# Optimization experiments

Hardware: AMD Instinct MI355X
Metric: run time of the kernel (lower is better)

The kernel has to match this reference:

```python
import jax, jax.numpy as jnp
import numpy as np

H = 16        # num_attention_heads
G = 16        # groups
SCALE_MIN = 0.95
SCALE_MAX = 1.05


def setup_inputs() -> dict:
    key = jax.random.key(0)
    ks = jax.random.split(key, 9)
    B, S, E = 2, 2048, 1024
    d = {
        'hidden_states': jax.random.normal(ks[0], (B, S, E), jnp.float32),
        'Wq': jax.random.normal(ks[1], (E, E), jnp.float32) * (E ** -0.5),
        'bq': jax.random.normal(ks[2], (E,), jnp.float32) * 0.02,
        'Wk': jax.random.normal(ks[3], (E, E), jnp.float32) * (E ** -0.5),
        'bk': jax.random.normal(ks[4], (E,), jnp.float32) * 0.02,
        'Wv': jax.random.normal(ks[5], (E, E), jnp.float32) * (E ** -0.5),
        'bv': jax.random.normal(ks[6], (E,), jnp.float32) * 0.02,
        'Ws': jax.random.normal(ks[7], (H * G, E), jnp.float32) * (E ** -0.5),
        'bs': jax.random.normal(ks[8], (H * G,), jnp.float32) * 0.02,
    }
    return d


def _shape_heads(x, B, S):
    # [B,S,h*D] -> [B,h,S,D]
    return x.reshape(B, S, H, -1).transpose(0, 2, 1, 3)


def reference(hidden_states, Wq, bq, Wk, bk, Wv, bv, Ws, bs):
    B, S, E = hidden_states.shape
    D = E // H            # head dim = 64
    gd = D // G           # group dim = 4

    Q = _shape_heads(hidden_states @ Wq.T + bq, B, S)   # [B,h,S,D]
    K = _shape_heads(hidden_states @ Wk.T + bk, B, S)
    V = _shape_heads(hidden_states @ Wv.T + bv, B, S)

    # groupwise dynamic scales, narrow sigmoid range
    s_logits = hidden_states @ Ws.T + bs                 # [B,S,h*g]
    s = jax.nn.sigmoid(s_logits) * (SCALE_MAX - SCALE_MIN) + SCALE_MIN
    s = s.reshape(B, S, H, G).transpose(0, 2, 1, 3)      # [B,h,S,g]
    s = jnp.repeat(s, gd, axis=-1)                       # [B,h,S,D]

    Q = Q * s  # apply_to='q'

    scores = jnp.einsum('bhsd,bhtd->bhst', Q, K) / jnp.sqrt(jnp.float32(D))
    probs = jax.nn.softmax(scores, axis=-1)
    ctx = jnp.einsum('bhst,bhtd->bhsd', probs, V)        # [B,h,S,D]
    ctx = ctx.transpose(0, 2, 1, 3).reshape(B, S, H * D)
    return ctx
```

## Files before the change

### kernel.cpp

```cpp
#include <hip/hip_runtime.h>

typedef short bf16x8 __attribute__((ext_vector_type(8)));
typedef float f32x4 __attribute__((ext_vector_type(4)));

__device__ inline float bf2f(ushort u) {
    unsigned v = ((unsigned)u) << 16;
    return __builtin_bit_cast(float, v);
}
__device__ inline ushort f2bf(float f) {
    unsigned u = __builtin_bit_cast(unsigned, f);
    u += 0x7fffu + ((u >> 16) & 1u);
    return (ushort)(u >> 16);
}
__device__ inline void async_load16(const ushort* g, ushort* l) {
    __builtin_amdgcn_global_load_lds((const __attribute__((address_space(1))) void*)g,
                                     (__attribute__((address_space(3))) void*)l, 16, 0, 0);
}

__global__ void cast_all(const float* __restrict__ hs, const float* __restrict__ Wq,
                         const float* __restrict__ Wk, const float* __restrict__ Wv,
                         const float* __restrict__ Ws,
                         ushort* __restrict__ dhs, ushort* __restrict__ dWq,
                         ushort* __restrict__ dWk, ushort* __restrict__ dWv,
                         ushort* __restrict__ dWs)
{
    int bid = blockIdx.x;
    const float* src; ushort* dst; int off;
    if (bid < 2048)      { src = hs; dst = dhs; off = bid; }
    else if (bid < 2560) { src = Wq; dst = dWq; off = bid - 2048; }
    else if (bid < 3072) { src = Wk; dst = dWk; off = bid - 2560; }
    else if (bid < 3584) { src = Wv; dst = dWv; off = bid - 3072; }
    else                 { src = Ws; dst = dWs; off = bid - 3584; }
    int i = (off * 256 + threadIdx.x) * 8;
    float4 a = *(const float4*)(src + i);
    float4 b = *(const float4*)(src + i + 4);
    union { ushort u[8]; float4 v; } o;
    o.u[0] = f2bf(a.x); o.u[1] = f2bf(a.y); o.u[2] = f2bf(a.z); o.u[3] = f2bf(a.w);
    o.u[4] = f2bf(b.x); o.u[5] = f2bf(b.y); o.u[6] = f2bf(b.z); o.u[7] = f2bf(b.w);
    *(float4*)(dst + i) = o.v;
}

__launch_bounds__(256, 4)
__global__ void fused_qkvs(const ushort* __restrict__ X,
                           const ushort* __restrict__ Wq, const ushort* __restrict__ Wk,
                           const ushort* __restrict__ Wv, const ushort* __restrict__ Ws,
                           const float* __restrict__ bq, const float* __restrict__ bk,
                           const float* __restrict__ bv, const float* __restrict__ bs,
                           ushort* __restrict__ Qb, ushort* __restrict__ Kb,
                           ushort* __restrict__ VtG, float* __restrict__ sb)
{
    __shared__ __align__(16) ushort Sm[128 * 136];
    ushort* As = Sm;
    ushort* Bs = Sm + 128 * 64;

    const int tid = threadIdx.x, w = tid >> 6, lane = tid & 63;
    const int l15 = lane & 15, quad = lane >> 4;
    const int lrow = lane >> 3;
    const int gchunk = ((lane & 7) ^ lrow) * 8;

    const int wid = blockIdx.x;
    const int r8 = wid & 7, jj = wid >> 3;
    const int by = (jj & 3) * 8 + r8;
    const int xb = jj >> 2;
    const int m0 = by * 128;

    const ushort* W; const float* bias; int n0, mode;
    if (xb < 8)       { W = Wq; bias = bq; n0 = xb * 128;        mode = 1; }
    else if (xb < 16) { W = Wk; bias = bk; n0 = (xb - 8) * 128;  mode = 0; }
    else if (xb < 24) { W = Wv; bias = bv; n0 = (xb - 16) * 128; mode = 2; }
    else              { W = Ws; bias = bs; n0 = (xb - 24) * 128; mode = 3; }

    const int wm = (w >> 1) * 64, wn = (w & 1) * 64;

    f32x4 acc[4][4];
    for (int i = 0; i < 4; i++) for (int j = 0; j < 4; j++) acc[i][j] = (f32x4){0.f, 0.f, 0.f, 0.f};

    for (int k0 = 0; k0 < 1024; k0 += 64) {
        __syncthreads();
        for (int c = 0; c < 4; ++c) {
            int r = w * 32 + c * 8;
            async_load16(&X[(size_t)(m0 + r + lrow) * 1024 + k0 + gchunk], &As[r * 64]);
            async_load16(&W[(size_t)(n0 + r + lrow) * 1024 + k0 + gchunk], &Bs[r * 64]);
        }
        __syncthreads();
        for (int kk = 0; kk < 64; kk += 32) {
            const int csw = quad + (kk >> 3);
            bf16x8 a[4], b[4];
            for (int i = 0; i < 4; i++)
                a[i] = *(const bf16x8*)&As[(wm + i * 16 + l15) * 64 + ((csw ^ (l15 & 7)) * 8)];
            for (int j = 0; j < 4; j++)
                b[j] = *(const bf16x8*)&Bs[(wn + j * 16 + l15) * 64 + ((csw ^ (l15 & 7)) * 8)];
            for (int i = 0; i < 4; i++)
                for (int j = 0; j < 4; j++)
                    acc[i][j] = __builtin_amdgcn_mfma_f32_16x16x32_bf16(a[i], b[j], acc[i][j], 0, 0, 0);
        }
    }

    const float QSCALE = 0.125f * 1.44269504f;

    if (mode == 3) {
        for (int i = 0; i < 4; i++)
            for (int j = 0; j < 4; j++) {
                int gn = n0 + wn + j * 16 + l15;
                float bv_ = bias[gn];
                for (int r = 0; r < 4; r++) {
                    int gm = m0 + wm + i * 16 + quad * 4 + r;
                    float v = acc[i][j][r] + bv_;
                    float sg = __builtin_amdgcn_rcpf(1.0f + __builtin_amdgcn_exp2f(-v * 1.44269504f));
                    sb[(size_t)gm * 256 + gn] = sg * 0.1f + 0.95f;
                }
            }
        return;
    }

    __syncthreads();

    if (mode == 2) {
        for (int i = 0; i < 4; i++)
            for (int j = 0; j < 4; j++) {
                int gnl = wn + j * 16 + l15;
                float bv_ = bias[n0 + gnl];
                ushort4 pk;
                pk.x = f2bf(acc[i][j][0] + bv_);
                pk.y = f2bf(acc[i][j][1] + bv_);
                pk.z = f2bf(acc[i][j][2] + bv_);
                pk.w = f2bf(acc[i][j][3] + bv_);
                *(ushort4*)&Sm[gnl * 136 + wm + i * 16 + quad * 4] = pk;
            }
        __syncthreads();
        const int bb = m0 >> 11, sloc = m0 & 2047;
        for (int it = 0; it < 8; ++it) {
            int d = (tid >> 4) + it * 16;
            int s8 = (tid & 15) * 8;
            float4 v = *(float4*)&Sm[d * 136 + s8];
            int h = (n0 + d) >> 6, dd = d & 63;
            *(float4*)&VtG[(size_t)(bb * 16 + h) * 131072 + (size_t)dd * 2048 + sloc + s8] = v;
        }
    } else {
        for (int i = 0; i < 4; i++)
            for (int j = 0; j < 4; j++) {
                int gnl = wn + j * 16 + l15;
                float bv_ = bias[n0 + gnl];
                for (int r = 0; r < 4; r++) {
                    float v = acc[i][j][r] + bv_;
                    if (mode == 1) v *= QSCALE;
                    Sm[(wm + i * 16 + quad * 4 + r) * 136 + gnl] = f2bf(v);
                }
            }
        __syncthreads();
        ushort* dst = (mode == 1) ? Qb : Kb;
        for (int it = 0; it < 8; ++it) {
            int row = (tid >> 4) + it * 16, c = (tid & 15) * 8;
            *(float4*)&dst[(size_t)(m0 + row) * 1024 + n0 + c] = *(float4*)&Sm[row * 136 + c];
        }
    }
}

__launch_bounds__(128, 2)
__global__ void attn_kernel(const ushort* __restrict__ Q, const ushort* __restrict__ K,
                            const ushort* __restrict__ Vt, const float* __restrict__ sb,
                            float* __restrict__ out)
{
    __shared__ __align__(16) ushort SmA[4 * 4096];
    __shared__ __align__(16) ushort Ps[2048];
    ushort* Ks0 = SmA;
    ushort* Ks1 = SmA + 4096;
    ushort* Vs0 = SmA + 8192;
    ushort* Vs1 = SmA + 12288;
    ushort* Qs  = SmA + 4096;

    const int tid = threadIdx.x, w = tid >> 6, lane = tid & 63;
    const int l15 = lane & 15, quad = lane >> 4;
    const int lrow = lane >> 3;
    const int gchunk = ((lane & 7) ^ lrow) * 8;

    const int wid = blockIdx.x;
    const int r8 = wid & 7, jj = wid >> 3;
    const int bh = (jj & 3) * 8 + r8;
    const int qx = jj >> 2;
    const int b = bh >> 4, h = bh & 15;
    const int q0 = qx * 64;
    const size_t rowbase = (size_t)b * 2048;
    const int cbase = h * 64;

    const ushort* kg = K + (rowbase + w * 32 + lrow) * 1024 + cbase + gchunk;
    const ushort* vg = Vt + (size_t)bh * 131072 + (size_t)(w * 32 + lrow) * 2048 + gchunk;

    for (int c = 0; c < 4; ++c) {
        async_load16(kg + c * 8192,  Ks0 + w * 2048 + c * 512);
        async_load16(vg + c * 16384, Vs0 + w * 2048 + c * 512);
    }

    for (int it = 0; it < 4; ++it) {
        int l = tid + it * 128;
        int r = l >> 3, ch = l & 7;
        int c = ch * 8;
        union { float4 f; ushort u[8]; } uu, oo;
        uu.f = *(const float4*)&Q[(rowbase + q0 + r) * 1024 + cbase + c];
        const float* sp = &sb[(rowbase + q0 + r) * 256 + ((cbase + c) >> 2)];
        float s0 = sp[0], s1 = sp[1];
        for (int j = 0; j < 4; j++) oo.u[j] = f2bf(bf2f(uu.u[j]) * s0);
        for (int j = 4; j < 8; j++) oo.u[j] = f2bf(bf2f(uu.u[j]) * s1);
        *(float4*)&Qs[r * 64 + ((ch ^ (r & 7)) * 8)] = oo.f;
    }
    __syncthreads();

    bf16x8 aq[2][2];
    for (int mt = 0; mt < 2; mt++)
        for (int kk2 = 0; kk2 < 2; kk2++)
            aq[mt][kk2] = *(const bf16x8*)&Qs[(w * 32 + mt * 16 + l15) * 64
                                              + (((kk2 * 4 + quad) ^ (l15 & 7)) * 8)];

    int kvoff[2][4];
    for (int kk2 = 0; kk2 < 2; kk2++)
        for (int nt = 0; nt < 4; nt++)
            kvoff[kk2][nt] = (nt * 16 + l15) * 64 + (((quad + kk2 * 4) ^ (l15 & 7)) * 8);
    int wroff2[4], rdoff2[2];
    {
        const int base = w * 1024 + l15 * 64;
        for (int kt2 = 0; kt2 < 4; kt2++)
            wroff2[kt2] = base + (quad & 1) * 4 + (((kt2 * 2 + (quad >> 1)) ^ (l15 & 7)) * 8);
        for (int half = 0; half < 2; half++)
            rdoff2[half] = base + (((half * 4 + quad) ^ (l15 & 7)) * 8);
    }

    const bf16x8 vones = {0x3F80, 0x3F80, 0x3F80, 0x3F80, 0x3F80, 0x3F80, 0x3F80, 0x3F80};

    f32x4 osum[2];
    f32x4 o[2][4];
    for (int mt = 0; mt < 2; mt++) {
        osum[mt] = (f32x4){0.f, 0.f, 0.f, 0.f};
        for (int nt = 0; nt < 4; nt++) o[mt][nt] = (f32x4){0.f, 0.f, 0.f, 0.f};
    }
    const f32x4 z4 = (f32x4){0.f, 0.f, 0.f, 0.f};

#define ATTN_STEP(KC, VC, KN, VN, KT, PREFETCH)                                                         \
    {                                                                                                   \
        __syncthreads();                  \
        if (PREFETCH) {                                                                                 \
            const int nk = (KT) + 1;                                                                    \
            for (int c = 0; c < 4; ++c) {                                                               \
                async_load16(kg + nk * 65536 + c * 8192, KN + w * 2048 + c * 512);                      \
                async_load16(vg + nk * 64 + c * 16384,   VN + w * 2048 + c * 512);                      \
            }                                                                                           \
        }                                                                                               \
        bf16x8 kb[2][4], vb[2][4];                                                                      \
        for (int kk2 = 0; kk2 < 2; kk2++)                                                               \
            for (int nt = 0; nt < 4; nt++) {                                                            \
                kb[kk2][nt] = *(const bf16x8*)&KC[kvoff[kk2][nt]];                                      \
                vb[kk2][nt] = *(const bf16x8*)&VC[kvoff[kk2][nt]];                                      \
            }                                                                                           \
        for (int mt = 0; mt < 2; mt++) {                                                                \
                                                     \
            f32x4 st[4];                                                                                \
            __builtin_amdgcn_s_setprio(1);                                                              \
            for (int kt2 = 0; kt2 < 4; kt2++) {                                                         \
                st[kt2] = __builtin_amdgcn_mfma_f32_16x16x32_bf16(kb[0][kt2], aq[mt][0], z4, 0, 0, 0);  \
                st[kt2] = __builtin_amdgcn_mfma_f32_16x16x32_bf16(kb[1][kt2], aq[mt][1], st[kt2],       \
                                                                  0, 0, 0);                             \
            }                                                                                           \
            __builtin_amdgcn_s_setprio(0);                                                              \
            for (int kt2 = 0; kt2 < 4; kt2++) {                                                         \
                float p0 = __builtin_amdgcn_exp2f(st[kt2][0]);                                          \
                float p1 = __builtin_amdgcn_exp2f(st[kt2][1]);                                          \
                float p2 = __builtin_amdgcn_exp2f(st[kt2][2]);                                          \
                float p3 = __builtin_amdgcn_exp2f(st[kt2][3]);                                          \
                unsigned d0 = __builtin_amdgcn_perm(__builtin_bit_cast(unsigned, p1) + 0x8000u,         \
                                                    __builtin_bit_cast(unsigned, p0) + 0x8000u,         \
                                                    0x07060302u);                                       \
                unsigned d1 = __builtin_amdgcn_perm(__builtin_bit_cast(unsigned, p3) + 0x8000u,         \
                                                    __builtin_bit_cast(unsigned, p2) + 0x8000u,         \
                                                    0x07060302u);                                       \
                uint2 pk; pk.x = d0; pk.y = d1;                                                         \
                *(uint2*)&Ps[wroff2[kt2]] = pk;                                                         \
            }                                                                                           \
                           \
            __builtin_amdgcn_s_setprio(1);                                                              \
            for (int half = 0; half < 2; half++) {                                                      \
                bf16x8 a_ = *(const bf16x8*)&Ps[rdoff2[half]];                                          \
                osum[mt] = __builtin_amdgcn_mfma_f32_16x16x32_bf16(a_, vones, osum[mt], 0, 0, 0);       \
                for (int nt = 0; nt < 4; nt++)                                                          \
                    o[mt][nt] = __builtin_amdgcn_mfma_f32_16x16x32_bf16(a_, vb[half][nt],               \
                                                                        o[mt][nt], 0, 0, 0);            \
            }                                                                                           \
            __builtin_amdgcn_s_setprio(0);                                                              \
        }                                                                                               \
    }

    for (int kt = 0; kt < 32; kt += 2) {
        ATTN_STEP(Ks0, Vs0, Ks1, Vs1, kt, 1);
        ATTN_STEP(Ks1, Vs1, Ks0, Vs0, kt + 1, (kt + 2 < 32));
    }
#undef ATTN_STEP

    for (int mt = 0; mt < 2; mt++) {
        for (int r = 0; r < 4; r++) {
            float iv = __builtin_amdgcn_rcpf(osum[mt][r]);
            int q = q0 + w * 32 + mt * 16 + quad * 4 + r;
            size_t base = (rowbase + q) * 1024 + cbase;
            for (int nt = 0; nt < 4; nt++)
                out[base + nt * 16 + l15] = o[mt][nt][r] * iv;
        }
    }
}

extern "C" void kernel_launch(void* const* d_in, const int* in_sizes, int n_in,
                              void* d_out, int out_size, void* d_ws, size_t ws_size,
                              hipStream_t stream) {
    const float* hs = (const float*)d_in[0];
    const float* Wq = (const float*)d_in[1];
    const float* bq = (const float*)d_in[2];
    const float* Wk = (const float*)d_in[3];
    const float* bk = (const float*)d_in[4];
    const float* Wv = (const float*)d_in[5];
    const float* bv = (const float*)d_in[6];
    const float* Ws = (const float*)d_in[7];
    const float* bs = (const float*)d_in[8];
    float* outp = (float*)d_out;

    char* ws = (char*)d_ws;
    ushort* Qb    = (ushort*)(ws);
    ushort* Kb    = (ushort*)(ws + 8388608);
    ushort* VtG   = (ushort*)(ws + 16777216);
    float*  sb    = (float* )(ws + 25165824);
    ushort* hs_bf = (ushort*)(ws + 29360128);
    ushort* Wq_bf = (ushort*)(ws + 37748736);
    ushort* Wk_bf = (ushort*)(ws + 39845888);
    ushort* Wv_bf = (ushort*)(ws + 41943040);
    ushort* Ws_bf = (ushort*)(ws + 44040192);

    cast_all<<<dim3(3712), dim3(256), 0, stream>>>(hs, Wq, Wk, Wv, Ws,
                                                   hs_bf, Wq_bf, Wk_bf, Wv_bf, Ws_bf);
    fused_qkvs<<<dim3(832), dim3(256), 0, stream>>>(hs_bf, Wq_bf, Wk_bf, Wv_bf, Ws_bf,
                                                    bq, bk, bv, bs, Qb, Kb, VtG, sb);
    attn_kernel<<<dim3(1024), dim3(128), 0, stream>>>(Qb, Kb, VtG, sb, outp);
}
```

Baseline: 171.5 us.

## Load V fragments directly from global into registers, drop V LDS staging

```diff
diff --git a/kernel.cpp b/kernel.cpp
--- a/kernel.cpp
+++ b/kernel.cpp
@@ -161,12 +161,10 @@
                             const ushort* __restrict__ Vt, const float* __restrict__ sb,
                             float* __restrict__ out)
 {
-    __shared__ __align__(16) ushort SmA[4 * 4096];
+    __shared__ __align__(16) ushort SmA[2 * 4096];
     __shared__ __align__(16) ushort Ps[2048];
     ushort* Ks0 = SmA;
     ushort* Ks1 = SmA + 4096;
-    ushort* Vs0 = SmA + 8192;
-    ushort* Vs1 = SmA + 12288;
     ushort* Qs  = SmA + 4096;
 
     const int tid = threadIdx.x, w = tid >> 6, lane = tid & 63;
@@ -184,12 +182,16 @@
     const int cbase = h * 64;
 
     const ushort* kg = K + (rowbase + w * 32 + lrow) * 1024 + cbase + gchunk;
-    const ushort* vg = Vt + (size_t)bh * 131072 + (size_t)(w * 32 + lrow) * 2048 + gchunk;
-
-    for (int c = 0; c < 4; ++c) {
-        async_load16(kg + c * 8192,  Ks0 + w * 2048 + c * 512);
-        async_load16(vg + c * 16384, Vs0 + w * 2048 + c * 512);
-    }
+    const ushort* vgr = Vt + (size_t)bh * 131072 + (size_t)l15 * 2048 + quad * 8;
+
+    for (int c = 0; c < 4; ++c)
+        async_load16(kg + c * 8192, Ks0 + w * 2048 + c * 512);
+    bf16x8 vbA[2][4], vbB[2][4];
+#pragma unroll
+    for (int kk2 = 0; kk2 < 2; kk2++)
+#pragma unroll
+        for (int nt = 0; nt < 4; nt++)
+            vbA[kk2][nt] = *(const bf16x8*)(vgr + nt * 32768 + kk2 * 32);
 
     for (int it = 0; it < 4; ++it) {
         int l = tid + it * 128;
@@ -234,32 +236,31 @@
     }
     const f32x4 z4 = (f32x4){0.f, 0.f, 0.f, 0.f};
 
-#define ATTN_STEP(KC, VC, KN, VN, KT, PREFETCH)                                                         \
+#define ATTN_STEP(KC, KN, VB_CUR, VB_NXT, KT, PREFETCH)                                                 \
     {                                                                                                   \
-        __syncthreads();                  \
+        __syncthreads();                      \
         if (PREFETCH) {                                                                                 \
             const int nk = (KT) + 1;                                                                    \
-            for (int c = 0; c < 4; ++c) {                                                               \
+            for (int c = 0; c < 4; ++c)                                                                 \
                 async_load16(kg + nk * 65536 + c * 8192, KN + w * 2048 + c * 512);                      \
-                async_load16(vg + nk * 64 + c * 16384,   VN + w * 2048 + c * 512);                      \
-            }                                                                                           \
+            _Pragma("unroll")                                                                           \
+            for (int kk2 = 0; kk2 < 2; kk2++)                                                           \
+                _Pragma("unroll")                                                                       \
+                for (int nt = 0; nt < 4; nt++)                                                          \
+                    VB_NXT[kk2][nt] = *(const bf16x8*)(vgr + nk * 64 + nt * 32768 + kk2 * 32);          \
         }                                                                                               \
-        bf16x8 kb[2][4], vb[2][4];                                                                      \
+        bf16x8 kb[2][4];                                                                                \
         for (int kk2 = 0; kk2 < 2; kk2++)                                                               \
-            for (int nt = 0; nt < 4; nt++) {                                                            \
+            for (int nt = 0; nt < 4; nt++)                                                              \
                 kb[kk2][nt] = *(const bf16x8*)&KC[kvoff[kk2][nt]];                                      \
-                vb[kk2][nt] = *(const bf16x8*)&VC[kvoff[kk2][nt]];                                      \
-            }                                                                                           \
         for (int mt = 0; mt < 2; mt++) {                                                                \
                                                      \
             f32x4 st[4];                                                                                \
-            __builtin_amdgcn_s_setprio(1);                                                              \
             for (int kt2 = 0; kt2 < 4; kt2++) {                                                         \
                 st[kt2] = __builtin_amdgcn_mfma_f32_16x16x32_bf16(kb[0][kt2], aq[mt][0], z4, 0, 0, 0);  \
                 st[kt2] = __builtin_amdgcn_mfma_f32_16x16x32_bf16(kb[1][kt2], aq[mt][1], st[kt2],       \
                                                                   0, 0, 0);                             \
             }                                                                                           \
-            __builtin_amdgcn_s_setprio(0);                                                              \
             for (int kt2 = 0; kt2 < 4; kt2++) {                                                         \
                 float p0 = __builtin_amdgcn_exp2f(st[kt2][0]);                                          \
                 float p1 = __builtin_amdgcn_exp2f(st[kt2][1]);                                          \
@@ -275,21 +276,19 @@
                 *(uint2*)&Ps[wroff2[kt2]] = pk;                                                         \
             }                                                                                           \
                            \
-            __builtin_amdgcn_s_setprio(1);                                                              \
             for (int half = 0; half < 2; half++) {                                                      \
                 bf16x8 a_ = *(const bf16x8*)&Ps[rdoff2[half]];                                          \
                 osum[mt] = __builtin_amdgcn_mfma_f32_16x16x32_bf16(a_, vones, osum[mt], 0, 0, 0);       \
                 for (int nt = 0; nt < 4; nt++)                                                          \
-                    o[mt][nt] = __builtin_amdgcn_mfma_f32_16x16x32_bf16(a_, vb[half][nt],               \
+                    o[mt][nt] = __builtin_amdgcn_mfma_f32_16x16x32_bf16(a_, VB_CUR[half][nt],           \
                                                                         o[mt][nt], 0, 0, 0);            \
             }                                                                                           \
-            __builtin_amdgcn_s_setprio(0);                                                              \
         }                                                                                               \
     }
 
     for (int kt = 0; kt < 32; kt += 2) {
-        ATTN_STEP(Ks0, Vs0, Ks1, Vs1, kt, 1);
-        ATTN_STEP(Ks1, Vs1, Ks0, Vs0, kt + 1, (kt + 2 < 32));
+        ATTN_STEP(Ks0, Ks1, vbA, vbB, kt, 1);
+        ATTN_STEP(Ks1, Ks0, vbB, vbA, kt + 1, (kt + 2 < 32));
     }
 #undef ATTN_STEP
 
```

Result: slower. 191.9 us (+11.9%).

## Split attention work across four waves of sixteen query rows each

Applied to the files above, without the earlier changes.

```diff
diff --git a/kernel.cpp b/kernel.cpp
--- a/kernel.cpp
+++ b/kernel.cpp
@@ -156,13 +156,13 @@
     }
 }
 
-__launch_bounds__(128, 2)
+__launch_bounds__(256, 4)
 __global__ void attn_kernel(const ushort* __restrict__ Q, const ushort* __restrict__ K,
                             const ushort* __restrict__ Vt, const float* __restrict__ sb,
                             float* __restrict__ out)
 {
     __shared__ __align__(16) ushort SmA[4 * 4096];
-    __shared__ __align__(16) ushort Ps[2048];
+    __shared__ __align__(16) ushort Ps[4096];
     ushort* Ks0 = SmA;
     ushort* Ks1 = SmA + 4096;
     ushort* Vs0 = SmA + 8192;
@@ -183,16 +183,16 @@
     const size_t rowbase = (size_t)b * 2048;
     const int cbase = h * 64;
 
-    const ushort* kg = K + (rowbase + w * 32 + lrow) * 1024 + cbase + gchunk;
-    const ushort* vg = Vt + (size_t)bh * 131072 + (size_t)(w * 32 + lrow) * 2048 + gchunk;
-
-    for (int c = 0; c < 4; ++c) {
-        async_load16(kg + c * 8192,  Ks0 + w * 2048 + c * 512);
-        async_load16(vg + c * 16384, Vs0 + w * 2048 + c * 512);
-    }
-
-    for (int it = 0; it < 4; ++it) {
-        int l = tid + it * 128;
+    const ushort* kg = K + (rowbase + w * 16 + lrow) * 1024 + cbase + gchunk;
+    const ushort* vg = Vt + (size_t)bh * 131072 + (size_t)(w * 16 + lrow) * 2048 + gchunk;
+
+    for (int c = 0; c < 2; ++c) {
+        async_load16(kg + c * 8192,  Ks0 + w * 1024 + c * 512);
+        async_load16(vg + c * 16384, Vs0 + w * 1024 + c * 512);
+    }
+
+    for (int it = 0; it < 2; ++it) {
+        int l = tid + it * 256;
         int r = l >> 3, ch = l & 7;
         int c = ch * 8;
         union { float4 f; ushort u[8]; } uu, oo;
@@ -205,11 +205,10 @@
     }
     __syncthreads();
 
-    bf16x8 aq[2][2];
-    for (int mt = 0; mt < 2; mt++)
-        for (int kk2 = 0; kk2 < 2; kk2++)
-            aq[mt][kk2] = *(const bf16x8*)&Qs[(w * 32 + mt * 16 + l15) * 64
-                                              + (((kk2 * 4 + quad) ^ (l15 & 7)) * 8)];
+    bf16x8 aq[2];
+    for (int kk2 = 0; kk2 < 2; kk2++)
+        aq[kk2] = *(const bf16x8*)&Qs[(w * 16 + l15) * 64
+                                      + (((kk2 * 4 + quad) ^ (l15 & 7)) * 8)];
 
     int kvoff[2][4];
     for (int kk2 = 0; kk2 < 2; kk2++)
@@ -226,12 +225,9 @@
 
     const bf16x8 vones = {0x3F80, 0x3F80, 0x3F80, 0x3F80, 0x3F80, 0x3F80, 0x3F80, 0x3F80};
 
-    f32x4 osum[2];
-    f32x4 o[2][4];
-    for (int mt = 0; mt < 2; mt++) {
-        osum[mt] = (f32x4){0.f, 0.f, 0.f, 0.f};
-        for (int nt = 0; nt < 4; nt++) o[mt][nt] = (f32x4){0.f, 0.f, 0.f, 0.f};
-    }
+    f32x4 osum = (f32x4){0.f, 0.f, 0.f, 0.f};
+    f32x4 o[4];
+    for (int nt = 0; nt < 4; nt++) o[nt] = (f32x4){0.f, 0.f, 0.f, 0.f};
     const f32x4 z4 = (f32x4){0.f, 0.f, 0.f, 0.f};
 
 #define ATTN_STEP(KC, VC, KN, VN, KT, PREFETCH)                                                         \
@@ -239,51 +235,47 @@
         __syncthreads();                  \
         if (PREFETCH) {                                                                                 \
             const int nk = (KT) + 1;                                                                    \
-            for (int c = 0; c < 4; ++c) {                                                               \
-                async_load16(kg + nk * 65536 + c * 8192, KN + w * 2048 + c * 512);                      \
-                async_load16(vg + nk * 64 + c * 16384,   VN + w * 2048 + c * 512);                      \
+            for (int c = 0; c < 2; ++c) {                                                               \
+                async_load16(kg + nk * 65536 + c * 8192, KN + w * 1024 + c * 512);                      \
+                async_load16(vg + nk * 64 + c * 16384,   VN + w * 1024 + c * 512);                      \
             }                                                                                           \
         }                                                                                               \
-        bf16x8 kb[2][4], vb[2][4];                                                                      \
+        bf16x8 kb[2][4];                                                                                \
         for (int kk2 = 0; kk2 < 2; kk2++)                                                               \
-            for (int nt = 0; nt < 4; nt++) {                                                            \
+            for (int nt = 0; nt < 4; nt++)                                                              \
                 kb[kk2][nt] = *(const bf16x8*)&KC[kvoff[kk2][nt]];                                      \
+                                                     \
+        f32x4 st[4];                                                                                    \
+        for (int kt2 = 0; kt2 < 4; kt2++) {                                                             \
+            st[kt2] = __builtin_amdgcn_mfma_f32_16x16x32_bf16(kb[0][kt2], aq[0], z4, 0, 0, 0);          \
+            st[kt2] = __builtin_amdgcn_mfma_f32_16x16x32_bf16(kb[1][kt2], aq[1], st[kt2], 0, 0, 0);     \
+        }                                                                                               \
+                                     \
+        bf16x8 vb[2][4];                                                                                \
+        for (int kk2 = 0; kk2 < 2; kk2++)                                                               \
+            for (int nt = 0; nt < 4; nt++)                                                              \
                 vb[kk2][nt] = *(const bf16x8*)&VC[kvoff[kk2][nt]];                                      \
-            }                                                                                           \
-        for (int mt = 0; mt < 2; mt++) {                                                                \
-                                                     \
-            f32x4 st[4];                                                                                \
-            __builtin_amdgcn_s_setprio(1);                                                              \
-            for (int kt2 = 0; kt2 < 4; kt2++) {                                                         \
-                st[kt2] = __builtin_amdgcn_mfma_f32_16x16x32_bf16(kb[0][kt2], aq[mt][0], z4, 0, 0, 0);  \
-                st[kt2] = __builtin_amdgcn_mfma_f32_16x16x32_bf16(kb[1][kt2], aq[mt][1], st[kt2],       \
-                                                                  0, 0, 0);                             \
-            }                                                                                           \
-            __builtin_amdgcn_s_setprio(0);                                                              \
-            for (int kt2 = 0; kt2 < 4; kt2++) {                                                         \
-                float p0 = __builtin_amdgcn_exp2f(st[kt2][0]);                                          \
-                float p1 = __builtin_amdgcn_exp2f(st[kt2][1]);                                          \
-                float p2 = __builtin_amdgcn_exp2f(st[kt2][2]);                                          \
-                float p3 = __builtin_amdgcn_exp2f(st[kt2][3]);                                          \
-                unsigned d0 = __builtin_amdgcn_perm(__builtin_bit_cast(unsigned, p1) + 0x8000u,         \
-                                                    __builtin_bit_cast(unsigned, p0) + 0x8000u,         \
-                                                    0x07060302u);                                       \
-                unsigned d1 = __builtin_amdgcn_perm(__builtin_bit_cast(unsigned, p3) + 0x8000u,         \
-                                                    __builtin_bit_cast(unsigned, p2) + 0x8000u,         \
-                                                    0x07060302u);                                       \
-                uint2 pk; pk.x = d0; pk.y = d1;                                                         \
-                *(uint2*)&Ps[wroff2[kt2]] = pk;                                                         \
-            }                                                                                           \
-                           \
-            __builtin_amdgcn_s_setprio(1);                                                              \
-            for (int half = 0; half < 2; half++) {                                                      \
-                bf16x8 a_ = *(const bf16x8*)&Ps[rdoff2[half]];                                          \
-                osum[mt] = __builtin_amdgcn_mfma_f32_16x16x32_bf16(a_, vones, osum[mt], 0, 0, 0);       \
-                for (int nt = 0; nt < 4; nt++)                                                          \
-                    o[mt][nt] = __builtin_amdgcn_mfma_f32_16x16x32_bf16(a_, vb[half][nt],               \
-                                                                        o[mt][nt], 0, 0, 0);            \
-            }                                                                                           \
-            __builtin_amdgcn_s_setprio(0);                                                              \
+        for (int kt2 = 0; kt2 < 4; kt2++) {                                                             \
+            float p0 = __builtin_amdgcn_exp2f(st[kt2][0]);                                              \
+            float p1 = __builtin_amdgcn_exp2f(st[kt2][1]);                                              \
+            float p2 = __builtin_amdgcn_exp2f(st[kt2][2]);                                              \
+            float p3 = __builtin_amdgcn_exp2f(st[kt2][3]);                                              \
+            unsigned d0 = __builtin_amdgcn_perm(__builtin_bit_cast(unsigned, p1) + 0x8000u,             \
+                                                __builtin_bit_cast(unsigned, p0) + 0x8000u,             \
+                                                0x07060302u);                                           \
+            unsigned d1 = __builtin_amdgcn_perm(__builtin_bit_cast(unsigned, p3) + 0x8000u,             \
+                                                __builtin_bit_cast(unsigned, p2) + 0x8000u,             \
+                                                0x07060302u);                                           \
+            uint2 pk; pk.x = d0; pk.y = d1;                                                             \
+            *(uint2*)&Ps[wroff2[kt2]] = pk;                                                             \
+        }                                                                                               \
+                      \
+        for (int half = 0; half < 2; half++) {                                                          \
+            bf16x8 a_ = *(const bf16x8*)&Ps[rdoff2[half]];                                              \
+            osum = __builtin_amdgcn_mfma_f32_16x16x32_bf16(a_, vones, osum, 0, 0, 0);                   \
+            for (int nt = 0; nt < 4; nt++)                                                              \
+                o[nt] = __builtin_amdgcn_mfma_f32_16x16x32_bf16(a_, vb[half][nt],                       \
+                                                                o[nt], 0, 0, 0);                        \
         }                                                                                               \
     }
 
@@ -293,14 +285,12 @@
     }
 #undef ATTN_STEP
 
-    for (int mt = 0; mt < 2; mt++) {
-        for (int r = 0; r < 4; r++) {
-            float iv = __builtin_amdgcn_rcpf(osum[mt][r]);
-            int q = q0 + w * 32 + mt * 16 + quad * 4 + r;
-            size_t base = (rowbase + q) * 1024 + cbase;
-            for (int nt = 0; nt < 4; nt++)
-                out[base + nt * 16 + l15] = o[mt][nt][r] * iv;
-        }
+    for (int r = 0; r < 4; r++) {
+        float iv = __builtin_amdgcn_rcpf(osum[r]);
+        int q = q0 + w * 16 + quad * 4 + r;
+        size_t base = (rowbase + q) * 1024 + cbase;
+        for (int nt = 0; nt < 4; nt++)
+            out[base + nt * 16 + l15] = o[nt][r] * iv;
     }
 }
 
@@ -333,5 +323,5 @@
                                                    hs_bf, Wq_bf, Wk_bf, Wv_bf, Ws_bf);
     fused_qkvs<<<dim3(832), dim3(256), 0, stream>>>(hs_bf, Wq_bf, Wk_bf, Wv_bf, Ws_bf,
                                                     bq, bk, bv, bs, Qb, Kb, VtG, sb);
-    attn_kernel<<<dim3(1024), dim3(128), 0, stream>>>(Qb, Kb, VtG, sb, outp);
-}
+    attn_kernel<<<dim3(1024), dim3(256), 0, stream>>>(Qb, Kb, VtG, sb, outp);
+}
```

Result: no change. 174.0 us (+1.4%).
